# Optimization experiments

Measured on AMD Instinct MI355X. Metric: run time of the kernel, lower is better.

Reference implementation:

```python
import jax, jax.numpy as jnp
import numpy as np

B, NL, NH, NG, NC, GOI = 1024, 64, 32, 20000, 64, 1000
EPS = 1e-5


def setup_inputs() -> dict:
    key = jax.random.key(0)
    ks = jax.random.split(key, 8)
    latent = jax.random.normal(ks[0], (B, NL), dtype=jnp.float32)
    genes_oi = jax.random.randint(ks[1], (GOI,), 0, NG, dtype=jnp.int64)
    W = jax.random.normal(ks[2], (NL, NH), dtype=jnp.float32) / np.sqrt(NL)
    b = jnp.zeros((NH,), dtype=jnp.float32)
    bn_gamma = jnp.ones((NH,), dtype=jnp.float32)
    bn_beta = jnp.zeros((NH,), dtype=jnp.float32)
    bn_mean = jnp.zeros((NH,), dtype=jnp.float32)
    bn_var = jnp.ones((NH,), dtype=jnp.float32)
    logit_table = jax.random.normal(ks[3], (NG, NH, NC), dtype=jnp.float32) * 0.02
    rho_table = jax.random.uniform(ks[4], (NG, NH), dtype=jnp.float32,
                                   minval=-1.0 / np.sqrt(NH), maxval=1.0 / np.sqrt(NH))
    return {"latent": latent, "genes_oi": genes_oi, "W": W, "b": b,
            "bn_gamma": bn_gamma, "bn_beta": bn_beta, "bn_mean": bn_mean,
            "bn_var": bn_var, "logit_table": logit_table, "rho_table": rho_table}


def reference(latent, genes_oi, W, b, bn_gamma, bn_beta, bn_mean, bn_var,
              logit_table, rho_table):
    # MLP: Linear -> BatchNorm1d (eval, running stats) -> ReLU (dropout off in eval)
    h = latent @ W + b                                      # [B, NH]
    h = (h - bn_mean) * jax.lax.rsqrt(bn_var + EPS) * bn_gamma + bn_beta
    h = jax.nn.relu(h)
    # sparse gather of per-gene weight tensors, then batched small matmul
    lw = logit_table[genes_oi]                              # [GOI, NH, NC]
    logit = jnp.einsum('bh,ghc->bgc', h, lw)                # [B, GOI, NC]
    rho = h @ rho_table.T                                   # [B, NG] (full weight)
    return (logit, rho)
```

## Files before the change

kernel.cpp:

```cpp
#include <hip/hip_runtime.h>

#define BATCH 1024
#define NL    64
#define NH    32
#define NG    20000
#define NC    64
#define GOI   1000

typedef __attribute__((ext_vector_type(8))) short  short8;
typedef __attribute__((ext_vector_type(4))) float  f32x4;

static __device__ __forceinline__ unsigned short f2bf(float f) {
    unsigned int u = __builtin_bit_cast(unsigned int, f);
    unsigned int r = (u + 0x7fffu + ((u >> 16) & 1u)) >> 16;
    return (unsigned short)r;
}

__global__ __launch_bounds__(256) void h_kernel(
    const float* __restrict__ latent,
    const float* __restrict__ W,
    const float* __restrict__ bias,
    const float* __restrict__ gamma,
    const float* __restrict__ beta,
    const float* __restrict__ mean,
    const float* __restrict__ var,
    unsigned short* __restrict__ h)
{
    int tid = blockIdx.x * 256 + threadIdx.x;
    int b = tid >> 5;
    int k = tid & 31;
    float acc = 0.f;
    #pragma unroll 8
    for (int j = 0; j < NL; ++j)
        acc += latent[b * NL + j] * W[j * NH + k];
    acc += bias[k];
    float x = (acc - mean[k]) * rsqrtf(var[k] + 1e-5f) * gamma[k] + beta[k];
    x = fmaxf(x, 0.f);
    h[tid] = f2bf(x);
}

__global__ __launch_bounds__(256) void logit_kernel(
    const unsigned short* __restrict__ h,
    const float*          __restrict__ table,
    const int*            __restrict__ genes,
    float*                __restrict__ out)
{
    const int g    = blockIdx.x;
    const int wave = threadIdx.x >> 6;
    const int lane = threadIdx.x & 63;
    const int l15  = lane & 15;
    const int quad = lane >> 4;

    const long long gene = (long long)genes[g];
    const float* lw = table + gene * (long long)(NH * NC);

    short8 bf[4];
    #pragma unroll
    for (int t = 0; t < 4; ++t) {
        #pragma unroll
        for (int j = 0; j < 8; ++j)
            bf[t][j] = (short)f2bf(lw[(quad * 8 + j) * NC + t * 16 + l15]);
    }

    #pragma unroll
    for (int it = 0; it < 4; ++it) {
        const int b0 = blockIdx.y * 256 + it * 64 + wave * 16;
        short8 af = *(const short8*)(h + (b0 + l15) * NH + quad * 8);
        #pragma unroll
        for (int t = 0; t < 4; ++t) {
            f32x4 acc = {0.f, 0.f, 0.f, 0.f};
            acc = __builtin_amdgcn_mfma_f32_16x16x32_bf16(af, bf[t], acc, 0, 0, 0);
            #pragma unroll
            for (int r = 0; r < 4; ++r) {
                int b = b0 + quad * 4 + r;
                out[((long long)b * GOI + g) * NC + t * 16 + l15] = acc[r];
            }
        }
    }
}

__global__ __launch_bounds__(256) void rho_kernel(
    const unsigned short* __restrict__ h,
    const float*          __restrict__ rtab,
    float*                __restrict__ out)
{
    const int ng   = blockIdx.x;
    const int wave = threadIdx.x >> 6;
    const int lane = threadIdx.x & 63;
    const int l15  = lane & 15;
    const int quad = lane >> 4;
    const int b0   = blockIdx.y * 64 + wave * 16;

    short8 af = *(const short8*)(h + (b0 + l15) * NH + quad * 8);

    #pragma unroll
    for (int t = 0; t < 4; ++t) {
        const int n0 = ng * 64 + t * 16;
        if (n0 >= NG) break;
        const float* rp = rtab + (long long)(n0 + l15) * NH + quad * 8;
        short8 bfr;
        #pragma unroll
        for (int j = 0; j < 8; ++j)
            bfr[j] = (short)f2bf(rp[j]);
        f32x4 acc = {0.f, 0.f, 0.f, 0.f};
        acc = __builtin_amdgcn_mfma_f32_16x16x32_bf16(af, bfr, acc, 0, 0, 0);
        #pragma unroll
        for (int r = 0; r < 4; ++r) {
            int b = b0 + quad * 4 + r;
            out[(long long)b * NG + n0 + l15] = acc[r];
        }
    }
}

extern "C" void kernel_launch(void* const* d_in, const int* in_sizes, int n_in,
                              void* d_out, int out_size, void* d_ws, size_t ws_size,
                              hipStream_t stream) {
    const float* latent = (const float*)d_in[0];
    const int*   genes  = (const int*)d_in[1];
    const float* W      = (const float*)d_in[2];
    const float* bias   = (const float*)d_in[3];
    const float* gamma  = (const float*)d_in[4];
    const float* beta   = (const float*)d_in[5];
    const float* mean   = (const float*)d_in[6];
    const float* var    = (const float*)d_in[7];
    const float* ltab   = (const float*)d_in[8];
    const float* rtab   = (const float*)d_in[9];

    float* out = (float*)d_out;
    unsigned short* h = (unsigned short*)d_ws;

    float* out_logit = out;
    float* out_rho   = out + (long long)BATCH * GOI * NC;

    h_kernel<<<dim3((BATCH * NH) / 256), 256, 0, stream>>>(
        latent, W, bias, gamma, beta, mean, var, h);

    logit_kernel<<<dim3(GOI, 4), 256, 0, stream>>>(h, ltab, genes, out_logit);

    rho_kernel<<<dim3((NG + 63) / 64, BATCH / 64), 256, 0, stream>>>(
        h, rtab, out_rho);
}
```

Baseline: 457.1 us.

## Fuse logit and rho kernels into one launch with four genes per block

Merges the logit and rho kernels into a single launch whose grid is split by block index into logit blocks and rho blocks. The logit blocks now handle four consecutive genes each, so every lane writes a contiguous 256-float row segment per batch row, and the h fragment is reused across four genes. This removes one kernel launch and the gap between the two write-bound phases, and makes the logit stores more contiguous. In exchange it raises register use from holding 16 B fragments and 16 accumulators, which may lower occupancy.

```diff
diff --git a/kernel.cpp b/kernel.cpp
--- a/kernel.cpp
+++ b/kernel.cpp
@@ -6,6 +6,12 @@
 #define NG    20000
 #define NC    64
 #define GOI   1000
+
+#define GPB          4
+#define LOGIT_BLOCKS ((GOI / GPB) * 4)
+#define RHO_NGRP     ((NG + 63) / 64)
+#define RHO_YB       (BATCH / 64)
+#define RHO_BLOCKS   (RHO_NGRP * RHO_YB)
 
 typedef __attribute__((ext_vector_type(8))) short  short8;
 typedef __attribute__((ext_vector_type(4))) float  f32x4;
@@ -39,75 +45,97 @@
     h[tid] = f2bf(x);
 }
 
-__global__ __launch_bounds__(256) void logit_kernel(
+__global__ __launch_bounds__(256) void main_kernel(
     const unsigned short* __restrict__ h,
-    const float*          __restrict__ table,
+    const float*          __restrict__ ltab,
     const int*            __restrict__ genes,
-    float*                __restrict__ out)
+    const float*          __restrict__ rtab,
+    float*                __restrict__ out_logit,
+    float*                __restrict__ out_rho)
 {
-    const int g    = blockIdx.x;
     const int wave = threadIdx.x >> 6;
     const int lane = threadIdx.x & 63;
     const int l15  = lane & 15;
     const int quad = lane >> 4;
+    const int bx   = blockIdx.x;
 
-    const long long gene = (long long)genes[g];
-    const float* lw = table + gene * (long long)(NH * NC);
+    if (bx < LOGIT_BLOCKS) {
+        const int gt  = bx >> 2;
+        const int ybl = bx & 3;
+        const int g0  = gt * GPB;
 
-    short8 bf[4];
-    #pragma unroll
-    for (int t = 0; t < 4; ++t) {
+        short8 bf[GPB][4];
         #pragma unroll
-        for (int j = 0; j < 8; ++j)
-            bf[t][j] = (short)f2bf(lw[(quad * 8 + j) * NC + t * 16 + l15]);
-    }
+        for (int g = 0; g < GPB; ++g) {
+            const long long gene = (long long)genes[g0 + g];
+            const float* lw = ltab + gene * (long long)(NH * NC);
+            #pragma unroll
+            for (int t = 0; t < 4; ++t) {
+                #pragma unroll
+                for (int j = 0; j < 8; ++j)
+                    bf[g][t][j] = (short)f2bf(lw[(quad * 8 + j) * NC + t * 16 + l15]);
+            }
+        }
 
-    #pragma unroll
-    for (int it = 0; it < 4; ++it) {
-        const int b0 = blockIdx.y * 256 + it * 64 + wave * 16;
+        #pragma unroll
+        for (int it = 0; it < 4; ++it) {
+            const int b0 = ybl * 256 + it * 64 + wave * 16;
+            short8 af = *(const short8*)(h + (b0 + l15) * NH + quad * 8);
+
+            f32x4 acc[GPB][4];
+            #pragma unroll
+            for (int g = 0; g < GPB; ++g) {
+                #pragma unroll
+                for (int t = 0; t < 4; ++t) {
+                    f32x4 z = {0.f, 0.f, 0.f, 0.f};
+                    acc[g][t] = __builtin_amdgcn_mfma_f32_16x16x32_bf16(af, bf[g][t], z, 0, 0, 0);
+                }
+            }
+
+            #pragma unroll
+            for (int r = 0; r < 4; ++r) {
+                const long long b = b0 + quad * 4 + r;
+                float* op = out_logit + (b * GOI + g0) * NC + l15;
+                #pragma unroll
+                for (int g = 0; g < GPB; ++g) {
+                    #pragma unroll
+                    for (int t = 0; t < 4; ++t)
+                        op[g * NC + t * 16] = acc[g][t][r];
+                }
+            }
+        }
+    } else {
+        const int rb = bx - LOGIT_BLOCKS;
+        const int yb = rb & 15;
+        const int ng = rb >> 4;
+        const int b0 = yb * 64 + wave * 16;
+
         short8 af = *(const short8*)(h + (b0 + l15) * NH + quad * 8);
+
+        f32x4 acc[4];
         #pragma unroll
         for (int t = 0; t < 4; ++t) {
-            f32x4 acc = {0.f, 0.f, 0.f, 0.f};
-            acc = __builtin_amdgcn_mfma_f32_16x16x32_bf16(af, bf[t], acc, 0, 0, 0);
-            #pragma unroll
-            for (int r = 0; r < 4; ++r) {
-                int b = b0 + quad * 4 + r;
-                out[((long long)b * GOI + g) * NC + t * 16 + l15] = acc[r];
+            const int n0 = ng * 64 + t * 16;
+            if (n0 < NG) {
+                const float* rp = rtab + (long long)(n0 + l15) * NH + quad * 8;
+                short8 bfr;
+                #pragma unroll
+                for (int j = 0; j < 8; ++j)
+                    bfr[j] = (short)f2bf(rp[j]);
+                f32x4 z = {0.f, 0.f, 0.f, 0.f};
+                acc[t] = __builtin_amdgcn_mfma_f32_16x16x32_bf16(af, bfr, z, 0, 0, 0);
             }
         }
-    }
-}
 
-__global__ __launch_bounds__(256) void rho_kernel(
-    const unsigned short* __restrict__ h,
-    const float*          __restrict__ rtab,
-    float*                __restrict__ out)
-{
-    const int ng   = blockIdx.x;
-    const int wave = threadIdx.x >> 6;
-    const int lane = threadIdx.x & 63;
-    const int l15  = lane & 15;
-    const int quad = lane >> 4;
-    const int b0   = blockIdx.y * 64 + wave * 16;
-
-    short8 af = *(const short8*)(h + (b0 + l15) * NH + quad * 8);
-
-    #pragma unroll
-    for (int t = 0; t < 4; ++t) {
-        const int n0 = ng * 64 + t * 16;
-        if (n0 >= NG) break;
-        const float* rp = rtab + (long long)(n0 + l15) * NH + quad * 8;
-        short8 bfr;
-        #pragma unroll
-        for (int j = 0; j < 8; ++j)
-            bfr[j] = (short)f2bf(rp[j]);
-        f32x4 acc = {0.f, 0.f, 0.f, 0.f};
-        acc = __builtin_amdgcn_mfma_f32_16x16x32_bf16(af, bfr, acc, 0, 0, 0);
         #pragma unroll
         for (int r = 0; r < 4; ++r) {
-            int b = b0 + quad * 4 + r;
-            out[(long long)b * NG + n0 + l15] = acc[r];
+            const long long b = b0 + quad * 4 + r;
+            float* op = out_rho + b * NG + ng * 64 + l15;
+            #pragma unroll
+            for (int t = 0; t < 4; ++t) {
+                if (ng * 64 + t * 16 < NG)
+                    op[t * 16] = acc[t][r];
+            }
         }
     }
 }
@@ -135,8 +163,6 @@
     h_kernel<<<dim3((BATCH * NH) / 256), 256, 0, stream>>>(
         latent, W, bias, gamma, beta, mean, var, h);
 
-    logit_kernel<<<dim3(GOI, 4), 256, 0, stream>>>(h, ltab, genes, out_logit);
-
-    rho_kernel<<<dim3((NG + 63) / 64, BATCH / 64), 256, 0, stream>>>(
-        h, rtab, out_rho);
+    main_kernel<<<dim3(LOGIT_BLOCKS + RHO_BLOCKS), 256, 0, stream>>>(
+        h, ltab, genes, rtab, out_logit, out_rho);
 }
```

Result: slower. 502.1 us (+9.8%).
